# Performance work log

Measured on AMD Instinct MI355X. Metric: run time of the kernel, lower is better.

## Reference

```python
import jax, jax.numpy as jnp
import numpy as np

NEG_SLOPE = 0.2
EPS = 1e-16  # PyG softmax denominator epsilon


def gatv2_conv(x, src, dst, Wl, bl, Wr, br, att, bias, concat):
    """PyG GATv2Conv: x [N,F]; src/dst [E] (self loops already appended)."""
    N = x.shape[0]
    H, C = att.shape
    xl = (x @ Wl + bl).reshape(N, H, C)  # source transform
    xr = (x @ Wr + br).reshape(N, H, C)  # target transform
    # per-edge message: LeakyReLU(x_l[j] + x_r[i]), scored by att vector
    m = jax.nn.leaky_relu(xl[src] + xr[dst], NEG_SLOPE)     # [E,H,C]
    e = jnp.einsum('ehc,hc->eh', m, att)                    # [E,H]
    # segment softmax over incoming edges of each target node
    emax = jax.ops.segment_max(e, dst, num_segments=N)      # [N,H]
    ex = jnp.exp(e - emax[dst])
    denom = jax.ops.segment_sum(ex, dst, num_segments=N)    # [N,H]
    alpha = ex / (denom[dst] + EPS)                         # [E,H]
    out = jax.ops.segment_sum(xl[src] * alpha[:, :, None], dst, num_segments=N)  # [N,H,C]
    if concat:
        return out.reshape(N, H * C) + bias
    return out.mean(axis=1) + bias


def setup_inputs() -> dict:
    key = jax.random.key(0)
    ks = jax.random.split(key, 16)
    NUM_GRAPHS, NUM_NODES = 64, 512
    N = NUM_GRAPHS * NUM_NODES            # 32768
    E = 262144                            # avg degree 8
    F_IN, H, C1, C2 = 512, 4, 128, 64

    x = jax.random.normal(ks[0], (N, F_IN), dtype=jnp.float32)

    # within-graph edges with no self loops
    e_per_g = E // NUM_GRAPHS
    src_local = jax.random.randint(ks[1], (E,), 0, NUM_NODES)
    off = jax.random.randint(ks[2], (E,), 1, NUM_NODES)
    dst_local = (src_local + off) % NUM_NODES
    gid = jnp.repeat(jnp.arange(NUM_GRAPHS), e_per_g)
    edge_index = jnp.stack([gid * NUM_NODES + src_local,
                            gid * NUM_NODES + dst_local]).astype(jnp.int64)

    def lin(k, fi, fo):
        s = 1.0 / np.sqrt(fi)
        return jax.random.uniform(k, (fi, fo), jnp.float32, -s, s)

    return {
        'x': x, 'edge_index': edge_index, 'num_graphs': NUM_GRAPHS,
        # layer 1: in 512 -> heads*128, concat
        'Wl1': lin(ks[3], F_IN, H * C1), 'bl1': jnp.zeros((H * C1,), jnp.float32),
        'Wr1': lin(ks[4], F_IN, H * C1), 'br1': jnp.zeros((H * C1,), jnp.float32),
        'att1': jax.random.normal(ks[5], (H, C1), jnp.float32) * 0.1,
        'bias1': jnp.zeros((H * C1,), jnp.float32),
        # layer 2: in 512 -> 64, mean over heads
        'Wl2': lin(ks[6], H * C1, H * C2), 'bl2': jnp.zeros((H * C2,), jnp.float32),
        'Wr2': lin(ks[7], H * C1, H * C2), 'br2': jnp.zeros((H * C2,), jnp.float32),
        'att2': jax.random.normal(ks[8], (H, C2), jnp.float32) * 0.1,
        'bias2': jnp.zeros((C2,), jnp.float32),
    }


def reference(x, edge_index, num_graphs, Wl1, bl1, Wr1, br1, att1, bias1,
              Wl2, bl2, Wr2, br2, att2, bias2):
    N = x.shape[0]
    num_nodes = N // num_graphs
    loops = jnp.arange(N, dtype=edge_index.dtype)
    src = jnp.concatenate([edge_index[0], loops])
    dst = jnp.concatenate([edge_index[1], loops])
    h = gatv2_conv(x, src, dst, Wl1, bl1, Wr1, br1, att1, bias1, concat=True)
    h = gatv2_conv(h, src, dst, Wl2, bl2, Wr2, br2, att2, bias2, concat=False)
    # view [G, num_nodes, C2], mean over feature dim (dim=2 in the original)
    out = h.reshape(num_graphs, num_nodes, -1).mean(axis=2)
    return out  # pretraining=True -> (x, None, None); return tensor only
```

## Files before the change

### kernel.cpp

```cpp
#include <hip/hip_runtime.h>
#include <hip/hip_bf16.h>


typedef __bf16 bf16_t;
typedef bf16_t bf16x8 __attribute__((ext_vector_type(8)));
typedef float f32x4 __attribute__((ext_vector_type(4)));
typedef unsigned short ushort8 __attribute__((ext_vector_type(8)));

__device__ __forceinline__ unsigned short f2bf_rn(float f) {
    unsigned u = __float_as_uint(f);
    unsigned r = (u + 0x7FFFu + ((u >> 16) & 1u)) >> 16;
    return (unsigned short)r;
}


__global__ void hist_kernel(const int* __restrict__ ei, int E, int N,
                            int* __restrict__ deg) {
    int total = E + N;
    for (int e = blockIdx.x * blockDim.x + threadIdx.x; e < total;
         e += gridDim.x * blockDim.x) {
        int dst = (e < E) ? ei[E + e] : (e - E);
        atomicAdd(&deg[dst], 1);
    }
}

__global__ __launch_bounds__(512) void scan_pg(const int* __restrict__ deg,
                                               int* __restrict__ off,
                                               int NPG, int EPG) {
    __shared__ int buf[512];
    int g = blockIdx.x, tid = threadIdx.x;
    int base = g * NPG;
    buf[tid] = deg[base + tid];
    __syncthreads();
    #pragma unroll
    for (int ofs = 1; ofs < 512; ofs <<= 1) {
        int t = (tid >= ofs) ? buf[tid - ofs] : 0;
        __syncthreads();
        buf[tid] += t;
        __syncthreads();
    }
    off[base + tid + 1] = g * EPG + buf[tid];
    if (tid == 0) off[base] = g * EPG;
}

__global__ void scatter_kernel(const int* __restrict__ ei, int E, int N,
                               const int* __restrict__ off, int* __restrict__ cnt,
                               int* __restrict__ csrc) {
    int total = E + N;
    for (int e = blockIdx.x * blockDim.x + threadIdx.x; e < total;
         e += gridDim.x * blockDim.x) {
        int src, dst;
        if (e < E) { src = ei[e]; dst = ei[E + e]; }
        else       { src = e - E; dst = e - E; }
        int pos = off[dst] + atomicAdd(&cnt[dst], 1);
        csrc[pos] = src;
    }
}


__global__ __launch_bounds__(256) void cast_hi_kernel(
        const float* __restrict__ X, unsigned short* __restrict__ hi, int n4) {
    for (int i = blockIdx.x * blockDim.x + threadIdx.x; i < n4;
         i += gridDim.x * blockDim.x) {
        float4 v = ((const float4*)X)[i];
        ushort4 h;
        h.x = f2bf_rn(v.x); h.y = f2bf_rn(v.y);
        h.z = f2bf_rn(v.z); h.w = f2bf_rn(v.w);
        ((ushort4*)hi)[i] = h;
    }
}

__global__ __launch_bounds__(256) void tcast_kernel(
        const float* __restrict__ W, unsigned short* __restrict__ th,
        int K, int Nc) {
    __shared__ float t[32][33];
    int bx = blockIdx.x, by = blockIdx.y;
    int lx = threadIdx.x & 31, ly = threadIdx.x >> 5;
    #pragma unroll
    for (int r = ly; r < 32; r += 8)
        t[r][lx] = W[(size_t)(by * 32 + r) * Nc + bx * 32 + lx];
    __syncthreads();
    #pragma unroll
    for (int r = ly; r < 32; r += 8)
        th[(size_t)(bx * 32 + r) * K + by * 32 + lx] = f2bf_rn(t[lx][r]);
}


__global__ __launch_bounds__(256) void gemm128b(
        const unsigned short* __restrict__ A,
        const unsigned short* __restrict__ B,
        const float* __restrict__ bias, unsigned short* __restrict__ C,
        int M, int K, int Nc) {
    constexpr int NQ  = 4;
    constexpr int BUF = 16384;
    __shared__ __align__(16) char smem[2 * BUF];

    int tid  = threadIdx.x;
    int wave = tid >> 6, lane = tid & 63;
    int wr = wave >> 1, wc = wave & 1;

    int bx = blockIdx.x, by = blockIdx.y;
    if ((gridDim.y & 7) == 0) {
        int d = blockIdx.y * gridDim.x + blockIdx.x;
        int x = d & 7, i = d >> 3;
        by = (i / gridDim.x) * 8 + x;
        bx = i % gridDim.x;
    }
    int m0 = by * 128, n0 = bx * 128;

    const unsigned short* gsrc[NQ];
    int loff[NQ];
    #pragma unroll
    for (int q = 0; q < NQ; ++q) {
        int o    = q * 4096 + tid * 16;
        int tile = o >> 13;
        int ot   = o & 8191;
        int row  = ot >> 6;
        int slot = (ot >> 4) & 3;
        int sl   = slot ^ ((row >> 1) & 3);
        const unsigned short* base =
            (tile == 0) ? (A + (size_t)(m0 + row) * K)
                        : (B + (size_t)(n0 + row) * K);
        gsrc[q] = base + sl * 8;
        loff[q] = q * 4096 + wave * 1024;
    }

    f32x4 acc[4][4];
    #pragma unroll
    for (int i = 0; i < 4; ++i)
        #pragma unroll
        for (int j = 0; j < 4; ++j) acc[i][j] = (f32x4){0.f, 0.f, 0.f, 0.f};

    int r = lane & 15, g = lane >> 4;
    int sw = (g ^ ((r >> 1) & 3)) * 16;

    #pragma unroll
    for (int q = 0; q < NQ; ++q) {
        __builtin_amdgcn_global_load_lds(
            (const __attribute__((address_space(1))) void*)(gsrc[q]),
            (__attribute__((address_space(3))) void*)(smem + loff[q]), 16, 0, 0);
        gsrc[q] += 32;
    }
    __syncthreads();

    const int NT = K >> 5;
    int cur = 0;
    for (int t = 0; t < NT; ++t) {
        if (t + 1 < NT) {
            #pragma unroll
            for (int q = 0; q < NQ; ++q) {
                __builtin_amdgcn_global_load_lds(
                    (const __attribute__((address_space(1))) void*)(gsrc[q]),
                    (__attribute__((address_space(3))) void*)(smem + loff[q] + (cur ^ BUF)),
                    16, 0, 0);
                gsrc[q] += 32;
            }
        }
        const char* sb = smem + cur;
        bf16x8 a[4], b[4];
        #pragma unroll
        for (int i = 0; i < 4; ++i) {
            int offA = (wr * 64 + i * 16 + r) * 64 + sw;
            int offB = (wc * 64 + i * 16 + r) * 64 + sw;
            a[i] = *(const bf16x8*)(sb + offA);
            b[i] = *(const bf16x8*)(sb + 8192 + offB);
        }
        __builtin_amdgcn_s_setprio(1);
        #pragma unroll
        for (int i = 0; i < 4; ++i)
            #pragma unroll
            for (int j = 0; j < 4; ++j)
                acc[i][j] = __builtin_amdgcn_mfma_f32_16x16x32_bf16(a[i], b[j], acc[i][j], 0, 0, 0);
        __builtin_amdgcn_s_setprio(0);
        __syncthreads();
        cur ^= BUF;
    }

    #pragma unroll
    for (int j = 0; j < 4; ++j) {
        int col = n0 + wc * 64 + j * 16 + r;
        float bv = bias[col];
        #pragma unroll
        for (int i = 0; i < 4; ++i) {
            int rowb = m0 + wr * 64 + i * 16 + g * 4;
            #pragma unroll
            for (int t = 0; t < 4; ++t)
                C[(size_t)(rowb + t) * Nc + col] = f2bf_rn(acc[i][j][t] + bv);
        }
    }
}


__device__ __forceinline__ int edge_blk_swz(int blk, int swz) {
    if (swz) {
        int x = blk & 7, i = blk >> 3;
        blk = (i >> 7) * 1024 + x * 128 + (i & 127);
    }
    return blk;
}


__global__ __launch_bounds__(256) void gat_edge1(
        const unsigned short* __restrict__ xlr,
        const float* __restrict__ att, const float* __restrict__ bias,
        const int* __restrict__ roff, const int* __restrict__ csrc,
        unsigned short* __restrict__ Hh, int chunkN, int n0, int swz) {
    int blk = edge_blk_swz(blockIdx.x, swz);
    int node = blk * 4 + (threadIdx.x >> 6);
    if (node >= chunkN) return;
    int lane = threadIdx.x & 63;
    int bc = lane * 8;
    float xrv[8], att6[8], att4[8];
    {
        uint4 t0 = *(const uint4*)&xlr[(size_t)node * 1024 + 512 + bc];
        const unsigned* u = (const unsigned*)&t0;
        #pragma unroll
        for (int j = 0; j < 4; ++j) {
            xrv[2*j]   = __uint_as_float(u[j] << 16);
            xrv[2*j+1] = __uint_as_float(u[j] & 0xFFFF0000u);
        }
        float4 a0 = *(const float4*)&att[bc];
        float4 a1 = *(const float4*)&att[bc + 4];
        float av[8] = {a0.x, a0.y, a0.z, a0.w, a1.x, a1.y, a1.z, a1.w};
        #pragma unroll
        for (int k = 0; k < 8; ++k) { att6[k] = 0.6f * av[k]; att4[k] = 0.4f * av[k]; }
    }
    float acc[8];
    float m = 0.0f, d = 0.0f;
    int e0 = roff[n0 + node], e1 = roff[n0 + node + 1];
    uint4 cv;
    {
        int s = csrc[e0] - n0;
        cv = *(const uint4*)&xlr[(size_t)s * 1024 + bc];
    }
    for (int e = e0; e < e1; ++e) {
        float xv[8];
        {
            const unsigned* u = (const unsigned*)&cv;
            #pragma unroll
            for (int j = 0; j < 4; ++j) {
                xv[2*j]   = __uint_as_float(u[j] << 16);
                xv[2*j+1] = __uint_as_float(u[j] & 0xFFFF0000u);
            }
        }
        if (e + 1 < e1) {
            int s2 = csrc[e + 1] - n0;
            cv = *(const uint4*)&xlr[(size_t)s2 * 1024 + bc];
        }
        float p = 0.0f;
        #pragma unroll
        for (int k = 0; k < 8; ++k) {
            float t = xv[k] + xrv[k];
            p = fmaf(att6[k], t, p);
            p = fmaf(att4[k], fabsf(t), p);
        }
        p += __shfl_xor(p, 1); p += __shfl_xor(p, 2);
        p += __shfl_xor(p, 4); p += __shfl_xor(p, 8);
        if (e == e0) {
            m = p; d = 1.0f;
            #pragma unroll
            for (int k = 0; k < 8; ++k) acc[k] = xv[k];
        } else if (p > m + 8.0f) {
            float sc = __expf(m - p);
            d = fmaf(d, sc, 1.0f);
            #pragma unroll
            for (int k = 0; k < 8; ++k) acc[k] = fmaf(acc[k], sc, xv[k]);
            m = p;
        } else {
            float w = __expf(p - m);
            d += w;
            #pragma unroll
            for (int k = 0; k < 8; ++k) acc[k] = fmaf(w, xv[k], acc[k]);
        }
    }
    float inv = 1.0f / d;
    ushort8 hv;
    #pragma unroll
    for (int k = 0; k < 8; ++k)
        ((unsigned short*)&hv)[k] = f2bf_rn(fmaf(acc[k], inv, bias[bc + k]));
    *(ushort8*)&Hh[(size_t)node * 512 + bc] = hv;
}


__global__ __launch_bounds__(256) void gat_edge2(
        const unsigned short* __restrict__ xlr,
        const float* __restrict__ att, const float* __restrict__ bias,
        const int* __restrict__ roff, const int* __restrict__ csrc,
        float* __restrict__ out, int chunkN, int n0, int swz) {
    int blk = edge_blk_swz(blockIdx.x, swz);
    int node = blk * 4 + (threadIdx.x >> 6);
    if (node >= chunkN) return;
    int lane = threadIdx.x & 63;
    int bc = lane * 4;
    float xrv[4], att6[4], att4[4];
    {
        uint2 t0 = *(const uint2*)&xlr[(size_t)node * 512 + 256 + bc];
        const unsigned* u = (const unsigned*)&t0;
        #pragma unroll
        for (int j = 0; j < 2; ++j) {
            xrv[2*j]   = __uint_as_float(u[j] << 16);
            xrv[2*j+1] = __uint_as_float(u[j] & 0xFFFF0000u);
        }
        float4 a0 = *(const float4*)&att[bc];
        float av[4] = {a0.x, a0.y, a0.z, a0.w};
        #pragma unroll
        for (int k = 0; k < 4; ++k) { att6[k] = 0.6f * av[k]; att4[k] = 0.4f * av[k]; }
    }
    float acc[4];
    float m = 0.0f, d = 0.0f;
    int e0 = roff[n0 + node], e1 = roff[n0 + node + 1];
    uint2 cv;
    {
        int s = csrc[e0] - n0;
        cv = *(const uint2*)&xlr[(size_t)s * 512 + bc];
    }
    for (int e = e0; e < e1; ++e) {
        float xv[4];
        {
            const unsigned* u = (const unsigned*)&cv;
            #pragma unroll
            for (int j = 0; j < 2; ++j) {
                xv[2*j]   = __uint_as_float(u[j] << 16);
                xv[2*j+1] = __uint_as_float(u[j] & 0xFFFF0000u);
            }
        }
        if (e + 1 < e1) {
            int s2 = csrc[e + 1] - n0;
            cv = *(const uint2*)&xlr[(size_t)s2 * 512 + bc];
        }
        float p = 0.0f;
        #pragma unroll
        for (int k = 0; k < 4; ++k) {
            float t = xv[k] + xrv[k];
            p = fmaf(att6[k], t, p);
            p = fmaf(att4[k], fabsf(t), p);
        }
        p += __shfl_xor(p, 1); p += __shfl_xor(p, 2);
        p += __shfl_xor(p, 4); p += __shfl_xor(p, 8);
        if (e == e0) {
            m = p; d = 1.0f;
            #pragma unroll
            for (int k = 0; k < 4; ++k) acc[k] = xv[k];
        } else if (p > m + 8.0f) {
            float sc = __expf(m - p);
            d = fmaf(d, sc, 1.0f);
            #pragma unroll
            for (int k = 0; k < 4; ++k) acc[k] = fmaf(acc[k], sc, xv[k]);
            m = p;
        } else {
            float w = __expf(p - m);
            d += w;
            #pragma unroll
            for (int k = 0; k < 4; ++k) acc[k] = fmaf(w, xv[k], acc[k]);
        }
    }
    float inv = 1.0f / d;
    float v[4];
    #pragma unroll
    for (int k = 0; k < 4; ++k) v[k] = acc[k] * inv;
    #pragma unroll
    for (int k = 0; k < 4; ++k) {
        v[k] += __shfl_xor(v[k], 16);
        v[k] += __shfl_xor(v[k], 32);
    }
    int cb = (lane & 15) * 4;
    float s = 0.25f * (v[0] + v[1] + v[2] + v[3])
            + bias[cb] + bias[cb + 1] + bias[cb + 2] + bias[cb + 3];
    s += __shfl_xor(s, 1); s += __shfl_xor(s, 2);
    s += __shfl_xor(s, 4); s += __shfl_xor(s, 8);
    if (lane == 0) out[node] = s * (1.0f / 64.0f);
}


extern "C" void kernel_launch(void* const* d_in, const int* in_sizes, int n_in,
                              void* d_out, int out_size, void* d_ws, size_t ws_size,
                              hipStream_t stream) {
    const float* x    = (const float*)d_in[0];
    const int*   ei   = (const int*)d_in[1];
    const float* Wl1  = (const float*)d_in[3];
    const float* bl1  = (const float*)d_in[4];
    const float* Wr1  = (const float*)d_in[5];
    const float* br1  = (const float*)d_in[6];
    const float* att1 = (const float*)d_in[7];
    const float* bias1= (const float*)d_in[8];
    const float* Wl2  = (const float*)d_in[9];
    const float* bl2  = (const float*)d_in[10];
    const float* Wr2  = (const float*)d_in[11];
    const float* br2  = (const float*)d_in[12];
    const float* att2 = (const float*)d_in[13];
    const float* bias2= (const float*)d_in[14];
    float* out = (float*)d_out;

    const int F = 512;
    const int N = in_sizes[0] / F;
    const int E = in_sizes[1] / 2;
    const int NG = 64;
    const int NPG = N / NG;
    const int EPG = E / NG + NPG;

    char* w = (char*)d_ws;
    int* roff = (int*)(w);
    int* cnt  = (int*)(w + 0x40000);
    int* csrc = (int*)(w + 0x80000);
    unsigned short* wc1 = (unsigned short*)(w + 0x200000);
    unsigned short* wc2 = (unsigned short*)(w + 0x400000);
    float* bcat1 = (float*)(w + 0x500000);
    float* bcat2 = (float*)(w + 0x501000);
    const size_t HDR = 6ull << 20;

    int chunkG = NG;
    while (chunkG > 1) {
        size_t need = HDR + 3ull * (size_t)chunkG * NPG * 512 * 4;
        if (need <= ws_size) break;
        chunkG >>= 1;
    }
    const int chunkN = chunkG * NPG;
    const size_t BSZ = (size_t)chunkN * 512 * 4;
    char* R1 = w + HDR;
    char* R2 = w + HDR + BSZ;
    const int swz = (chunkG % 8 == 0) ? 1 : 0;

    hipMemsetAsync(cnt, 0, (size_t)N * 4, stream);
    hist_kernel<<<1024, 256, 0, stream>>>(ei, E, N, cnt);
    scan_pg<<<NG, 512, 0, stream>>>(cnt, roff, NPG, EPG);
    hipMemsetAsync(cnt, 0, (size_t)N * 4, stream);
    scatter_kernel<<<1024, 256, 0, stream>>>(ei, E, N, roff, cnt, csrc);

    tcast_kernel<<<dim3(512/32, 512/32), 256, 0, stream>>>(Wl1, wc1, 512, 512);
    tcast_kernel<<<dim3(512/32, 512/32), 256, 0, stream>>>(Wr1, wc1 + 512*512, 512, 512);
    tcast_kernel<<<dim3(256/32, 512/32), 256, 0, stream>>>(Wl2, wc2, 512, 256);
    tcast_kernel<<<dim3(256/32, 512/32), 256, 0, stream>>>(Wr2, wc2 + 256*512, 512, 256);
    hipMemcpyAsync(bcat1,       bl1, 512 * 4, hipMemcpyDeviceToDevice, stream);
    hipMemcpyAsync(bcat1 + 512, br1, 512 * 4, hipMemcpyDeviceToDevice, stream);
    hipMemcpyAsync(bcat2,       bl2, 256 * 4, hipMemcpyDeviceToDevice, stream);
    hipMemcpyAsync(bcat2 + 256, br2, 256 * 4, hipMemcpyDeviceToDevice, stream);

    for (int g0 = 0; g0 < NG; g0 += chunkG) {
        int n0 = g0 * NPG;
        const float* xc = x + (size_t)n0 * 512;
        unsigned short* Xh   = (unsigned short*)R1;
        unsigned short* xlr1 = (unsigned short*)R2;
        unsigned short* Hh   = (unsigned short*)R1;
        unsigned short* xlr2 = (unsigned short*)R2;

        cast_hi_kernel<<<2048, 256, 0, stream>>>(xc, Xh, chunkN * 512 / 4);
        gemm128b<<<dim3(1024/128, chunkN/128), 256, 0, stream>>>(
            Xh, wc1, bcat1, xlr1, chunkN, 512, 1024);
        gat_edge1<<<(chunkN * 64) / 256, 256, 0, stream>>>(
            xlr1, att1, bias1, roff, csrc, Hh, chunkN, n0, swz);

        gemm128b<<<dim3(512/128, chunkN/128), 256, 0, stream>>>(
            Hh, wc2, bcat2, xlr2, chunkN, 512, 512);
        gat_edge2<<<(chunkN * 64) / 256, 256, 0, stream>>>(
            xlr2, att2, bias2, roff, csrc, out + n0, chunkN, n0, swz);
    }
}
```

Before: 206.7 us.

## Fuse CSR build into per-graph kernel and batch weight/bias prep launches

Replaces the global histogram, scan and scatter kernels (plus two memsets) with a single per-graph kernel that does the degree count, scan and scatter in shared memory. It relies on the input's layout: edges grouped contiguously by graph, 512 nodes per graph, and equal edge counts per graph. The four weight transpose-cast launches become one 3D launch, and the four bias memcpys become one small kernel. This removes many small launches and global atomics, but it runs only 64 blocks for the CSR build, which may serialize the edge scans.

```diff
diff --git a/kernel.cpp b/kernel.cpp
--- a/kernel.cpp
+++ b/kernel.cpp
@@ -14,23 +14,20 @@
 }
 
 
-__global__ void hist_kernel(const int* __restrict__ ei, int E, int N,
-                            int* __restrict__ deg) {
-    int total = E + N;
-    for (int e = blockIdx.x * blockDim.x + threadIdx.x; e < total;
-         e += gridDim.x * blockDim.x) {
-        int dst = (e < E) ? ei[E + e] : (e - E);
-        atomicAdd(&deg[dst], 1);
-    }
-}
-
-__global__ __launch_bounds__(512) void scan_pg(const int* __restrict__ deg,
-                                               int* __restrict__ off,
-                                               int NPG, int EPG) {
-    __shared__ int buf[512];
+__global__ __launch_bounds__(512) void csr_build(
+        const int* __restrict__ ei, int E, int NPG, int EPG_NL,
+        int* __restrict__ roff, int* __restrict__ csrc) {
+    __shared__ int deg[512], buf[512], soff[512], cnt[512];
     int g = blockIdx.x, tid = threadIdx.x;
-    int base = g * NPG;
-    buf[tid] = deg[base + tid];
+    int nb = g * NPG;
+    int eb = g * EPG_NL;
+    const int EPG = EPG_NL + NPG;
+    deg[tid] = 1;
+    __syncthreads();
+    for (int i = tid; i < EPG_NL; i += 512)
+        atomicAdd(&deg[ei[E + eb + i] - nb], 1);
+    __syncthreads();
+    buf[tid] = deg[tid];
     __syncthreads();
     #pragma unroll
     for (int ofs = 1; ofs < 512; ofs <<= 1) {
@@ -39,21 +36,18 @@
         buf[tid] += t;
         __syncthreads();
     }
-    off[base + tid + 1] = g * EPG + buf[tid];
-    if (tid == 0) off[base] = g * EPG;
-}
-
-__global__ void scatter_kernel(const int* __restrict__ ei, int E, int N,
-                               const int* __restrict__ off, int* __restrict__ cnt,
-                               int* __restrict__ csrc) {
-    int total = E + N;
-    for (int e = blockIdx.x * blockDim.x + threadIdx.x; e < total;
-         e += gridDim.x * blockDim.x) {
-        int src, dst;
-        if (e < E) { src = ei[e]; dst = ei[E + e]; }
-        else       { src = e - E; dst = e - E; }
-        int pos = off[dst] + atomicAdd(&cnt[dst], 1);
-        csrc[pos] = src;
+    int oe = buf[tid] - deg[tid];
+    soff[tid] = oe;
+    roff[nb + tid] = g * EPG + oe;
+    if (tid == 511) roff[nb + 512] = g * EPG + buf[511];
+    cnt[tid] = 1;
+    csrc[g * EPG + oe] = nb + tid;
+    __syncthreads();
+    for (int i = tid; i < EPG_NL; i += 512) {
+        int dl = ei[E + eb + i] - nb;
+        int s  = ei[eb + i];
+        int pos = atomicAdd(&cnt[dl], 1);
+        csrc[g * EPG + soff[dl] + pos] = s;
     }
 }
 
@@ -70,9 +64,17 @@
     }
 }
 
-__global__ __launch_bounds__(256) void tcast_kernel(
-        const float* __restrict__ W, unsigned short* __restrict__ th,
-        int K, int Nc) {
+__global__ __launch_bounds__(256) void tcast4_kernel(
+        const float* __restrict__ Wl1, const float* __restrict__ Wr1,
+        const float* __restrict__ Wl2, const float* __restrict__ Wr2,
+        unsigned short* __restrict__ wc1, unsigned short* __restrict__ wc2) {
+    int z = blockIdx.z;
+    int Nc = (z < 2) ? 512 : 256;
+    if (blockIdx.x * 32 >= Nc) return;
+    const float* W = (z == 0) ? Wl1 : (z == 1) ? Wr1 : (z == 2) ? Wl2 : Wr2;
+    unsigned short* th = (z == 0) ? wc1 : (z == 1) ? wc1 + 512 * 512
+                       : (z == 2) ? wc2 : wc2 + 256 * 512;
+    const int K = 512;
     __shared__ float t[32][33];
     int bx = blockIdx.x, by = blockIdx.y;
     int lx = threadIdx.x & 31, ly = threadIdx.x >> 5;
@@ -83,6 +85,17 @@
     #pragma unroll
     for (int r = ly; r < 32; r += 8)
         th[(size_t)(bx * 32 + r) * K + by * 32 + lx] = f2bf_rn(t[lx][r]);
+}
+
+__global__ __launch_bounds__(512) void bconcat_kernel(
+        const float* __restrict__ bl1, const float* __restrict__ br1,
+        const float* __restrict__ bl2, const float* __restrict__ br2,
+        float* __restrict__ bcat1, float* __restrict__ bcat2) {
+    int i = blockIdx.x * 512 + threadIdx.x;
+    if (i < 512)        bcat1[i] = bl1[i];
+    else if (i < 1024)  bcat1[i] = br1[i - 512];
+    else if (i < 1280)  bcat2[i - 1024] = bl2[i - 1024];
+    else if (i < 1536)  bcat2[i - 1024] = br2[i - 1280];
 }
 
 
@@ -396,11 +409,10 @@
     const int E = in_sizes[1] / 2;
     const int NG = 64;
     const int NPG = N / NG;
-    const int EPG = E / NG + NPG;
+    const int EPG_NL = E / NG;
 
     char* w = (char*)d_ws;
     int* roff = (int*)(w);
-    int* cnt  = (int*)(w + 0x40000);
     int* csrc = (int*)(w + 0x80000);
     unsigned short* wc1 = (unsigned short*)(w + 0x200000);
     unsigned short* wc2 = (unsigned short*)(w + 0x400000);
@@ -420,20 +432,9 @@
     char* R2 = w + HDR + BSZ;
     const int swz = (chunkG % 8 == 0) ? 1 : 0;
 
-    hipMemsetAsync(cnt, 0, (size_t)N * 4, stream);
-    hist_kernel<<<1024, 256, 0, stream>>>(ei, E, N, cnt);
-    scan_pg<<<NG, 512, 0, stream>>>(cnt, roff, NPG, EPG);
-    hipMemsetAsync(cnt, 0, (size_t)N * 4, stream);
-    scatter_kernel<<<1024, 256, 0, stream>>>(ei, E, N, roff, cnt, csrc);
-
-    tcast_kernel<<<dim3(512/32, 512/32), 256, 0, stream>>>(Wl1, wc1, 512, 512);
-    tcast_kernel<<<dim3(512/32, 512/32), 256, 0, stream>>>(Wr1, wc1 + 512*512, 512, 512);
-    tcast_kernel<<<dim3(256/32, 512/32), 256, 0, stream>>>(Wl2, wc2, 512, 256);
-    tcast_kernel<<<dim3(256/32, 512/32), 256, 0, stream>>>(Wr2, wc2 + 256*512, 512, 256);
-    hipMemcpyAsync(bcat1,       bl1, 512 * 4, hipMemcpyDeviceToDevice, stream);
-    hipMemcpyAsync(bcat1 + 512, br1, 512 * 4, hipMemcpyDeviceToDevice, stream);
-    hipMemcpyAsync(bcat2,       bl2, 256 * 4, hipMemcpyDeviceToDevice, stream);
-    hipMemcpyAsync(bcat2 + 256, br2, 256 * 4, hipMemcpyDeviceToDevice, stream);
+    csr_build<<<NG, 512, 0, stream>>>(ei, E, NPG, EPG_NL, roff, csrc);
+    tcast4_kernel<<<dim3(16, 16, 4), 256, 0, stream>>>(Wl1, Wr1, Wl2, Wr2, wc1, wc2);
+    bconcat_kernel<<<3, 512, 0, stream>>>(bl1, br1, bl2, br2, bcat1, bcat2);
 
     for (int g0 = 0; g0 < NG; g0 += chunkG) {
         int n0 = g0 * NPG;
```

Measured after the change: 176.6 us, median of 2. 1.17x faster.
